# Performance work log

Hardware: AMD Instinct MI355X
Metric: run time of the kernel (lower is better)

The kernel has to match this reference:

```python
import jax, jax.numpy as jnp
import numpy as np

N_UNITS = 524288
BATCH = 16384


def setup_inputs() -> dict:
    key = jax.random.key(0)
    ks = jax.random.split(key, 10)
    left_feats = jax.random.normal(ks[0], (N_UNITS, 9), dtype=jnp.float32)
    right_feats = jax.random.normal(ks[1], (N_UNITS, 9), dtype=jnp.float32)
    left_seg = jnp.sort(jax.random.randint(ks[2], (N_UNITS,), 0, BATCH, dtype=jnp.int32))
    right_seg = jnp.sort(jax.random.randint(ks[3], (N_UNITS,), 0, BATCH, dtype=jnp.int32))
    W1 = jax.random.normal(ks[4], (9, 64), dtype=jnp.float32) * (1.0 / np.sqrt(9))
    b1 = jax.random.normal(ks[5], (64,), dtype=jnp.float32) * 0.01
    Wc1 = jax.random.normal(ks[6], (128, 32), dtype=jnp.float32) * (1.0 / np.sqrt(128))
    bc1 = jax.random.normal(ks[7], (32,), dtype=jnp.float32) * 0.01
    Wc2 = jax.random.normal(ks[8], (32, 1), dtype=jnp.float32) * (1.0 / np.sqrt(32))
    bc2 = jax.random.normal(ks[9], (1,), dtype=jnp.float32) * 0.01
    return {"left_feats": left_feats, "right_feats": right_feats,
            "left_seg": left_seg, "right_seg": right_seg,
            "W1": W1, "b1": b1, "Wc1": Wc1, "bc1": bc1, "Wc2": Wc2, "bc2": bc2}


def _pooled_features(feats, seg, W1, b1):
    # per-unit MLP 9 -> 64 with ReLU, then ragged sum-pool per instance
    h = jax.nn.relu(feats @ W1 + b1)                      # [N, 64]
    return jax.ops.segment_sum(h, seg, num_segments=BATCH)  # [B, 64]


def reference(left_feats, right_feats, left_seg, right_seg, W1, b1, Wc1, bc1, Wc2, bc2):
    left = _pooled_features(left_feats, left_seg, W1, b1)    # [B, 64]
    right = _pooled_features(right_feats, right_seg, W1, b1)  # [B, 64]
    combined = jnp.concatenate([left, right], axis=1)         # [B, 128]
    hidden = jax.nn.relu(combined @ Wc1 + bc1)                # [B, 32]
    logits = hidden @ Wc2 + bc2                               # [B, 1]
    return jax.nn.sigmoid(jnp.squeeze(logits, axis=-1))       # [B]
```

## Files before the change

### kernel.cpp

```cpp
#include <hip/hip_runtime.h>
#include <math.h>

#define BATCH_C 16384
#define SPW 2

typedef float f32x4  __attribute__((ext_vector_type(4)));
typedef f32x4 __attribute__((aligned(4))) f32x4_u;
typedef float f32x16 __attribute__((ext_vector_type(16)));
typedef short s16x8  __attribute__((ext_vector_type(8)));

static __device__ inline unsigned rlo_f(float x) {
    unsigned u = __float_as_uint(x);
    return (u + 0x7fffu + ((u >> 16) & 1u)) >> 16;
}
static __device__ inline unsigned rhi_f(float x) {
    unsigned u = __float_as_uint(x);
    return (u + 0x7fffu + ((u >> 16) & 1u)) & 0xffff0000u;
}

__global__ __launch_bounds__(256) void seg_starts_kernel(
    const int* __restrict__ lseg, const int* __restrict__ rseg, int n,
    int* __restrict__ lstart, int* __restrict__ rstart)
{
    const int* __restrict__ seg = blockIdx.y ? rseg : lseg;
    int* __restrict__ start = blockIdx.y ? rstart : lstart;
    int i = blockIdx.x * blockDim.x + threadIdx.x;
    if (i >= n) return;
    int s = seg[i];
    int prev = (i == 0) ? -1 : seg[i - 1];
    for (int b = prev + 1; b <= s; ++b) start[b] = i;
    if (i == n - 1) {
        for (int b = s + 1; b <= BATCH_C; ++b) start[b] = n;
    }
}

__global__ __launch_bounds__(256, 4) void fused_kernel(
    const float* __restrict__ lfeats, const float* __restrict__ rfeats,
    const int* __restrict__ lstart, const int* __restrict__ rstart,
    const float* __restrict__ W1, const float* __restrict__ b1,
    const float* __restrict__ Wc1, const float* __restrict__ bc1,
    const float* __restrict__ Wc2, const float* __restrict__ bc2,
    float* __restrict__ out, int nunits)
{
    const int lane = threadIdx.x & 63;
    const int wv   = threadIdx.x >> 6;
    const int S0   = (blockIdx.x * 4 + wv) * SPW;
    const int r    = lane & 31;
    const int hh   = lane >> 5;

    __shared__ __align__(16) short sBh[2][32][16];
    __shared__ __align__(16) short sBl[2][32][16];
    __shared__ __align__(16) float sWT[32 * 132];
    __shared__ float sb2[32];
    __shared__ float sw2v[32];
    __shared__ __align__(16) float rowbuf[4][SPW][128];

    {
        const int t    = threadIdx.x;
        const int tile = t >> 7;
        const int col  = (t >> 2) & 31;
        const int k0   = (t & 3) * 4;
        const int ch   = tile * 32 + col;
#pragma unroll
        for (int q = 0; q < 4; ++q) {
            const int k = k0 + q;
            float v = 0.0f;
            if (k < 9) v = W1[k * 64 + ch];
            else if (k == 9) v = b1[ch];
            unsigned hi = rlo_f(v);
            float d = v - __uint_as_float(hi << 16);
            sBh[tile][col][k] = (short)hi;
            sBl[tile][col][k] = (short)rlo_f(d);
        }
    }
    for (int idx = threadIdx.x; idx < 128 * 32; idx += 256) {
        sWT[(idx & 31) * 132 + (idx >> 5)] = Wc1[idx];
    }
    if (threadIdx.x < 32) {
        sb2[threadIdx.x]  = bc1[threadIdx.x];
        sw2v[threadIdx.x] = Wc2[threadIdx.x];
    }
    __syncthreads();

    const s16x8 bh0 = *reinterpret_cast<const s16x8*>(&sBh[0][r][hh * 8]);
    const s16x8 bh1 = *reinterpret_cast<const s16x8*>(&sBh[1][r][hh * 8]);
    const s16x8 bl0 = *reinterpret_cast<const s16x8*>(&sBl[0][r][hh * 8]);
    const s16x8 bl1 = *reinterpret_cast<const s16x8*>(&sBl[1][r][hh * 8]);

    const int bidx = S0 + (lane <= SPW ? lane : SPW);
    const int svl = lstart[bidx];
    const int svr = rstart[bidx];

#define FETCH(POS, P0,P1,P2,P3,P4,P5,P6,P7) do {                          \
        int u_ = (POS) + r; if (u_ > nunits - 1) u_ = nunits - 1;         \
        const float* fp_ = feats + (size_t)u_ * 9;                        \
        if (hh == 0) {                                                    \
            f32x4 x0_ = *reinterpret_cast<const f32x4_u*>(fp_);           \
            f32x4 x1_ = *reinterpret_cast<const f32x4_u*>(fp_ + 4);       \
            P0 = x0_.x; P1 = x0_.y; P2 = x0_.z; P3 = x0_.w;               \
            P4 = x1_.x; P5 = x1_.y; P6 = x1_.z; P7 = x1_.w;               \
        } else {                                                          \
            P0 = fp_[8];                                                  \
        }                                                                 \
    } while (0)

#define WINBODY(CNT, P0,P1,P2,P3,P4,P5,P6,P7) do {                        \
    unsigned u0_ = __float_as_uint(P0), u1_ = __float_as_uint(P1);        \
    unsigned u2_ = __float_as_uint(P2), u3_ = __float_as_uint(P3);        \
    unsigned u4_ = __float_as_uint(P4), u5_ = __float_as_uint(P5);        \
    unsigned u6_ = __float_as_uint(P6), u7_ = __float_as_uint(P7);        \
    float d0_ = P0 - __uint_as_float(u0_ & 0xffff0000u);                  \
    float d1_ = P1 - __uint_as_float(u1_ & 0xffff0000u);                  \
    float d2_ = P2 - __uint_as_float(u2_ & 0xffff0000u);                  \
    float d3_ = P3 - __uint_as_float(u3_ & 0xffff0000u);                  \
    float d4_ = P4 - __uint_as_float(u4_ & 0xffff0000u);                  \
    float d5_ = P5 - __uint_as_float(u5_ & 0xffff0000u);                  \
    float d6_ = P6 - __uint_as_float(u6_ & 0xffff0000u);                  \
    float d7_ = P7 - __uint_as_float(u7_ & 0xffff0000u);                  \
    unsigned H01_ = (u0_ >> 16) | (u1_ & 0xffff0000u);                    \
    unsigned H23_ = (u2_ >> 16) | (u3_ & 0xffff0000u);                    \
    unsigned H45_ = (u4_ >> 16) | (u5_ & 0xffff0000u);                    \
    unsigned H67_ = (u6_ >> 16) | (u7_ & 0xffff0000u);                    \
    unsigned L01_ = rlo_f(d0_) | rhi_f(d1_);                              \
    unsigned L23_ = rlo_f(d2_) | rhi_f(d3_);                              \
    unsigned L45_ = rlo_f(d4_) | rhi_f(d5_);                              \
    unsigned L67_ = rlo_f(d6_) | rhi_f(d7_);                              \
    const bool val_  = (r < (CNT));                                       \
    const bool keep_ = val_ && (hh == 0);                                 \
    unsigned HH01_ = hh ? ((u0_ >> 16) | 0x3F800000u) : H01_;             \
    unsigned LL01_ = hh ? rlo_f(d0_) : L01_;                              \
    HH01_ = val_ ? HH01_ : 0u;                                            \
    LL01_ = val_ ? LL01_ : 0u;                                            \
    unsigned HH23_ = keep_ ? H23_ : 0u, HH45_ = keep_ ? H45_ : 0u;        \
    unsigned HH67_ = keep_ ? H67_ : 0u;                                   \
    unsigned LL23_ = keep_ ? L23_ : 0u, LL45_ = keep_ ? L45_ : 0u;        \
    unsigned LL67_ = keep_ ? L67_ : 0u;                                   \
    union { unsigned u[4]; s16x8 v; } Ah_, Al_;                           \
    Ah_.u[0] = HH01_; Ah_.u[1] = HH23_; Ah_.u[2] = HH45_; Ah_.u[3] = HH67_;\
    Al_.u[0] = LL01_; Al_.u[1] = LL23_; Al_.u[2] = LL45_; Al_.u[3] = LL67_;\
    if (posN < end_abs) { FETCH(posN, P0,P1,P2,P3,P4,P5,P6,P7); }         \
    posN = segadv(posN);                                                  \
    f32x16 cc0 = (f32x16)0.0f, cc1 = (f32x16)0.0f;                        \
    cc0 = __builtin_amdgcn_mfma_f32_32x32x16_bf16(Al_.v, bh0, cc0, 0,0,0);\
    cc0 = __builtin_amdgcn_mfma_f32_32x32x16_bf16(Ah_.v, bl0, cc0, 0,0,0);\
    cc0 = __builtin_amdgcn_mfma_f32_32x32x16_bf16(Ah_.v, bh0, cc0, 0,0,0);\
    cc1 = __builtin_amdgcn_mfma_f32_32x32x16_bf16(Al_.v, bh1, cc1, 0,0,0);\
    cc1 = __builtin_amdgcn_mfma_f32_32x32x16_bf16(Ah_.v, bl1, cc1, 0,0,0);\
    cc1 = __builtin_amdgcn_mfma_f32_32x32x16_bf16(Ah_.v, bh1, cc1, 0,0,0);\
    float s0_ = 0.0f, s1_ = 0.0f;                                         \
    _Pragma("unroll")                                                     \
    for (int t_ = 0; t_ < 16; ++t_) {                                     \
        s0_ += fmaxf(cc0[t_], 0.0f);                                      \
        s1_ += fmaxf(cc1[t_], 0.0f);                                      \
    }                                                                     \
    acc0 += s0_; acc1 += s1_;                                             \
} while (0)

    for (int side = 0; side < 2; ++side) {
        const float* __restrict__ feats = side ? rfeats : lfeats;
        const int sv = side ? svr : svl;
        const int s_abs = __shfl(sv, 0, 64);
        const int e1v = __shfl(sv, 1, 64);
        const int e2v = __shfl(sv, 2, 64);
        const int end_abs = e2v;

        auto segadv = [&](int p) -> int {
            int se = (p >= e1v) ? e2v : e1v;
            int w = se - p; if (w > 32) w = 32;
            return (p >= end_abs) ? p : (p + w);
        };

        float A0=0,A1=0,A2=0,A3=0,A4=0,A5=0,A6=0,A7=0;
        float B0=0,B1=0,B2=0,B3=0,B4=0,B5=0,B6=0,B7=0;
        const int pa = s_abs;
        if (pa < end_abs) FETCH(pa, A0,A1,A2,A3,A4,A5,A6,A7);
        const int pb = segadv(pa);
        if (pb < end_abs) FETCH(pb, B0,B1,B2,B3,B4,B5,B6,B7);
        int posN = segadv(pb);

        float acc0 = 0.0f, acc1 = 0.0f;
        int parity = 0;
        int base = s_abs;
        const int earr[SPW] = {e1v, e2v};

#pragma unroll
        for (int c = 0; c < SPW; ++c) {
            const int ec = earr[c];
            while (base < ec) {
                int cnt = ec - base; if (cnt > 32) cnt = 32;
                if (parity == 0) { WINBODY(cnt, A0,A1,A2,A3,A4,A5,A6,A7); }
                else             { WINBODY(cnt, B0,B1,B2,B3,B4,B5,B6,B7); }
                parity ^= 1;
                base += cnt;
            }
            acc0 += __shfl_xor(acc0, 32, 64);
            acc1 += __shfl_xor(acc1, 32, 64);
            rowbuf[wv][c][side * 64 + lane] = hh ? acc1 : acc0;
            acc0 = 0.0f; acc1 = 0.0f;
        }
    }
#undef WINBODY
#undef FETCH

    asm volatile("s_waitcnt lgkmcnt(0)" ::: "memory");

    {
        const int j = lane & 31;
        const float* __restrict__ rb = &rowbuf[wv][hh][0];
        const float* __restrict__ wt = &sWT[j * 132];

        float accA = sb2[j], accB = 0.0f;
#pragma unroll 8
        for (int q = 0; q < 32; ++q) {
            f32x4 v = *reinterpret_cast<const f32x4*>(rb + q * 4);
            f32x4 w = *reinterpret_cast<const f32x4*>(wt + q * 4);
            accA = fmaf(v.x, w.x, accA);
            accB = fmaf(v.y, w.y, accB);
            accA = fmaf(v.z, w.z, accA);
            accB = fmaf(v.w, w.w, accB);
        }
        float hsv = fmaxf(accA + accB, 0.0f) * sw2v[j];
#pragma unroll
        for (int off = 16; off > 0; off >>= 1) hsv += __shfl_xor(hsv, off, 64);

        if (j == 0) {
            float logit = hsv + bc2[0];
            out[S0 + hh] = 1.0f / (1.0f + expf(-logit));
        }
    }
}

extern "C" void kernel_launch(void* const* d_in, const int* in_sizes, int n_in,
                              void* d_out, int out_size, void* d_ws, size_t ws_size,
                              hipStream_t stream)
{
    const float* lfeats = (const float*)d_in[0];
    const float* rfeats = (const float*)d_in[1];
    const int*   lseg   = (const int*)d_in[2];
    const int*   rseg   = (const int*)d_in[3];
    const float* W1     = (const float*)d_in[4];
    const float* b1     = (const float*)d_in[5];
    const float* Wc1    = (const float*)d_in[6];
    const float* bc1    = (const float*)d_in[7];
    const float* Wc2    = (const float*)d_in[8];
    const float* bc2    = (const float*)d_in[9];
    float* out = (float*)d_out;

    const int n = in_sizes[2];

    int* lstart = (int*)d_ws;
    int* rstart = lstart + (BATCH_C + 16);

    seg_starts_kernel<<<dim3((n + 255) / 256, 2), 256, 0, stream>>>(
        lseg, rseg, n, lstart, rstart);

    fused_kernel<<<BATCH_C / (SPW * 4), 256, 0, stream>>>(
        lfeats, rfeats, lstart, rstart, W1, b1, Wc1, bc1, Wc2, bc2, out, n);
}
```

Before: 40.25 us.

## Interleave left and right segment streams and use branch-free unit fetch

The previous code processed the left side and then the right side, double-buffering fetches within each. The new loop runs both sides at once, so each iteration issues two independent fetch and MFMA chains to hide load latency. It also makes the fetch branch-free with a per-lane offset load, splits the ReLU reduction into several partial sums, and lowers the launch_bounds occupancy hint from 4 to 2 to give the compiler more registers. The trade-off is more register pressure, possibly fewer resident waves per CU, and extra handling for sides and empty segments.

```diff
diff --git a/kernel.cpp b/kernel.cpp
--- a/kernel.cpp
+++ b/kernel.cpp
@@ -8,6 +8,8 @@
 typedef f32x4 __attribute__((aligned(4))) f32x4_u;
 typedef float f32x16 __attribute__((ext_vector_type(16)));
 typedef short s16x8  __attribute__((ext_vector_type(8)));
+
+typedef union { unsigned u[4]; s16x8 v; } abfrag_t;
 
 static __device__ inline unsigned rlo_f(float x) {
     unsigned u = __float_as_uint(x);
@@ -34,7 +36,7 @@
     }
 }
 
-__global__ __launch_bounds__(256, 4) void fused_kernel(
+__global__ __launch_bounds__(256, 2) void fused_kernel(
     const float* __restrict__ lfeats, const float* __restrict__ rfeats,
     const int* __restrict__ lstart, const int* __restrict__ rstart,
     const float* __restrict__ W1, const float* __restrict__ b1,
@@ -47,6 +49,8 @@
     const int S0   = (blockIdx.x * 4 + wv) * SPW;
     const int r    = lane & 31;
     const int hh   = lane >> 5;
+    const int nmax = nunits - 1;
+    const int ofs1 = hh ? 5 : 4;
 
     __shared__ __align__(16) short sBh[2][32][16];
     __shared__ __align__(16) short sBl[2][32][16];
@@ -87,120 +91,131 @@
     const s16x8 bl0 = *reinterpret_cast<const s16x8*>(&sBl[0][r][hh * 8]);
     const s16x8 bl1 = *reinterpret_cast<const s16x8*>(&sBl[1][r][hh * 8]);
 
+    const f32x16 kZ = (f32x16)0.0f;
+
+    rowbuf[wv][0][lane] = 0.0f;  rowbuf[wv][0][64 + lane] = 0.0f;
+    rowbuf[wv][1][lane] = 0.0f;  rowbuf[wv][1][64 + lane] = 0.0f;
+
     const int bidx = S0 + (lane <= SPW ? lane : SPW);
     const int svl = lstart[bidx];
     const int svr = rstart[bidx];
-
-#define FETCH(POS, P0,P1,P2,P3,P4,P5,P6,P7) do {                          \
-        int u_ = (POS) + r; if (u_ > nunits - 1) u_ = nunits - 1;         \
-        const float* fp_ = feats + (size_t)u_ * 9;                        \
-        if (hh == 0) {                                                    \
-            f32x4 x0_ = *reinterpret_cast<const f32x4_u*>(fp_);           \
-            f32x4 x1_ = *reinterpret_cast<const f32x4_u*>(fp_ + 4);       \
-            P0 = x0_.x; P1 = x0_.y; P2 = x0_.z; P3 = x0_.w;               \
-            P4 = x1_.x; P5 = x1_.y; P6 = x1_.z; P7 = x1_.w;               \
-        } else {                                                          \
-            P0 = fp_[8];                                                  \
-        }                                                                 \
+    const int sLv = __shfl(svl, 0, 64);
+    const int e1L = __shfl(svl, 1, 64);
+    const int e2L = __shfl(svl, 2, 64);
+    const int sRv = __shfl(svr, 0, 64);
+    const int e1R = __shfl(svr, 1, 64);
+    const int e2R = __shfl(svr, 2, 64);
+    const int endL = e2L, endR = e2R;
+
+#define FETCH_(F, POS, Q0,Q1,Q2,Q3,Q4,Q5,Q6,Q7) do {                      \
+        int u_ = (POS) + r; if (u_ > nmax) u_ = nmax;                     \
+        const float* fp_ = (F) + (size_t)u_ * 9;                          \
+        f32x4 x0_ = *reinterpret_cast<const f32x4_u*>(fp_);               \
+        f32x4 x1_ = *reinterpret_cast<const f32x4_u*>(fp_ + ofs1);        \
+        Q0 = hh ? x1_.w : x0_.x;                                          \
+        Q1 = x0_.y; Q2 = x0_.z; Q3 = x0_.w;                               \
+        Q4 = x1_.x; Q5 = x1_.y; Q6 = x1_.z; Q7 = x1_.w;                   \
     } while (0)
 
-#define WINBODY(CNT, P0,P1,P2,P3,P4,P5,P6,P7) do {                        \
-    unsigned u0_ = __float_as_uint(P0), u1_ = __float_as_uint(P1);        \
-    unsigned u2_ = __float_as_uint(P2), u3_ = __float_as_uint(P3);        \
-    unsigned u4_ = __float_as_uint(P4), u5_ = __float_as_uint(P5);        \
-    unsigned u6_ = __float_as_uint(P6), u7_ = __float_as_uint(P7);        \
-    float d0_ = P0 - __uint_as_float(u0_ & 0xffff0000u);                  \
-    float d1_ = P1 - __uint_as_float(u1_ & 0xffff0000u);                  \
-    float d2_ = P2 - __uint_as_float(u2_ & 0xffff0000u);                  \
-    float d3_ = P3 - __uint_as_float(u3_ & 0xffff0000u);                  \
-    float d4_ = P4 - __uint_as_float(u4_ & 0xffff0000u);                  \
-    float d5_ = P5 - __uint_as_float(u5_ & 0xffff0000u);                  \
-    float d6_ = P6 - __uint_as_float(u6_ & 0xffff0000u);                  \
-    float d7_ = P7 - __uint_as_float(u7_ & 0xffff0000u);                  \
-    unsigned H01_ = (u0_ >> 16) | (u1_ & 0xffff0000u);                    \
-    unsigned H23_ = (u2_ >> 16) | (u3_ & 0xffff0000u);                    \
-    unsigned H45_ = (u4_ >> 16) | (u5_ & 0xffff0000u);                    \
-    unsigned H67_ = (u6_ >> 16) | (u7_ & 0xffff0000u);                    \
-    unsigned L01_ = rlo_f(d0_) | rhi_f(d1_);                              \
-    unsigned L23_ = rlo_f(d2_) | rhi_f(d3_);                              \
-    unsigned L45_ = rlo_f(d4_) | rhi_f(d5_);                              \
-    unsigned L67_ = rlo_f(d6_) | rhi_f(d7_);                              \
-    const bool val_  = (r < (CNT));                                       \
-    const bool keep_ = val_ && (hh == 0);                                 \
-    unsigned HH01_ = hh ? ((u0_ >> 16) | 0x3F800000u) : H01_;             \
-    unsigned LL01_ = hh ? rlo_f(d0_) : L01_;                              \
-    HH01_ = val_ ? HH01_ : 0u;                                            \
-    LL01_ = val_ ? LL01_ : 0u;                                            \
-    unsigned HH23_ = keep_ ? H23_ : 0u, HH45_ = keep_ ? H45_ : 0u;        \
-    unsigned HH67_ = keep_ ? H67_ : 0u;                                   \
-    unsigned LL23_ = keep_ ? L23_ : 0u, LL45_ = keep_ ? L45_ : 0u;        \
-    unsigned LL67_ = keep_ ? L67_ : 0u;                                   \
-    union { unsigned u[4]; s16x8 v; } Ah_, Al_;                           \
-    Ah_.u[0] = HH01_; Ah_.u[1] = HH23_; Ah_.u[2] = HH45_; Ah_.u[3] = HH67_;\
-    Al_.u[0] = LL01_; Al_.u[1] = LL23_; Al_.u[2] = LL45_; Al_.u[3] = LL67_;\
-    if (posN < end_abs) { FETCH(posN, P0,P1,P2,P3,P4,P5,P6,P7); }         \
-    posN = segadv(posN);                                                  \
-    f32x16 cc0 = (f32x16)0.0f, cc1 = (f32x16)0.0f;                        \
-    cc0 = __builtin_amdgcn_mfma_f32_32x32x16_bf16(Al_.v, bh0, cc0, 0,0,0);\
-    cc0 = __builtin_amdgcn_mfma_f32_32x32x16_bf16(Ah_.v, bl0, cc0, 0,0,0);\
-    cc0 = __builtin_amdgcn_mfma_f32_32x32x16_bf16(Ah_.v, bh0, cc0, 0,0,0);\
-    cc1 = __builtin_amdgcn_mfma_f32_32x32x16_bf16(Al_.v, bh1, cc1, 0,0,0);\
-    cc1 = __builtin_amdgcn_mfma_f32_32x32x16_bf16(Ah_.v, bl1, cc1, 0,0,0);\
-    cc1 = __builtin_amdgcn_mfma_f32_32x32x16_bf16(Ah_.v, bh1, cc1, 0,0,0);\
-    float s0_ = 0.0f, s1_ = 0.0f;                                         \
+#define CONV_(Q0,Q1,Q2,Q3,Q4,Q5,Q6,Q7, CNT, AH, AL) do {                  \
+    unsigned u0_=__float_as_uint(Q0), u1_=__float_as_uint(Q1),            \
+             u2_=__float_as_uint(Q2), u3_=__float_as_uint(Q3),            \
+             u4_=__float_as_uint(Q4), u5_=__float_as_uint(Q5),            \
+             u6_=__float_as_uint(Q6), u7_=__float_as_uint(Q7);            \
+    float d0_=Q0-__uint_as_float(u0_&0xffff0000u);                        \
+    float d1_=Q1-__uint_as_float(u1_&0xffff0000u);                        \
+    float d2_=Q2-__uint_as_float(u2_&0xffff0000u);                        \
+    float d3_=Q3-__uint_as_float(u3_&0xffff0000u);                        \
+    float d4_=Q4-__uint_as_float(u4_&0xffff0000u);                        \
+    float d5_=Q5-__uint_as_float(u5_&0xffff0000u);                        \
+    float d6_=Q6-__uint_as_float(u6_&0xffff0000u);                        \
+    float d7_=Q7-__uint_as_float(u7_&0xffff0000u);                        \
+    unsigned h01_=(u0_>>16)|(hh?0x3F800000u:(u1_&0xffff0000u));           \
+    unsigned l01_=rlo_f(d0_)|(hh?0u:rhi_f(d1_));                          \
+    unsigned h23_=(u2_>>16)|(u3_&0xffff0000u);                            \
+    unsigned h45_=(u4_>>16)|(u5_&0xffff0000u);                            \
+    unsigned h67_=(u6_>>16)|(u7_&0xffff0000u);                            \
+    unsigned l23_=rlo_f(d2_)|rhi_f(d3_);                                  \
+    unsigned l45_=rlo_f(d4_)|rhi_f(d5_);                                  \
+    unsigned l67_=rlo_f(d6_)|rhi_f(d7_);                                  \
+    const bool v_ = (r < (CNT));                                          \
+    const bool k_ = v_ && (hh == 0);                                      \
+    AH.u[0]=v_?h01_:0u; AL.u[0]=v_?l01_:0u;                               \
+    AH.u[1]=k_?h23_:0u; AL.u[1]=k_?l23_:0u;                               \
+    AH.u[2]=k_?h45_:0u; AL.u[2]=k_?l45_:0u;                               \
+    AH.u[3]=k_?h67_:0u; AL.u[3]=k_?l67_:0u;                               \
+} while (0)
+
+#define MFMAEPI_(AH, AL, A0, A1) do {                                     \
+    f32x16 c0_ = __builtin_amdgcn_mfma_f32_32x32x16_bf16(AL.v, bh0, kZ, 0,0,0); \
+    c0_ = __builtin_amdgcn_mfma_f32_32x32x16_bf16(AH.v, bl0, c0_, 0,0,0); \
+    c0_ = __builtin_amdgcn_mfma_f32_32x32x16_bf16(AH.v, bh0, c0_, 0,0,0); \
+    f32x16 c1_ = __builtin_amdgcn_mfma_f32_32x32x16_bf16(AL.v, bh1, kZ, 0,0,0); \
+    c1_ = __builtin_amdgcn_mfma_f32_32x32x16_bf16(AH.v, bl1, c1_, 0,0,0); \
+    c1_ = __builtin_amdgcn_mfma_f32_32x32x16_bf16(AH.v, bh1, c1_, 0,0,0); \
+    float sA_=0.f,sB_=0.f,sC_=0.f,sD_=0.f,tA_=0.f,tB_=0.f,tC_=0.f,tD_=0.f;\
     _Pragma("unroll")                                                     \
-    for (int t_ = 0; t_ < 16; ++t_) {                                     \
-        s0_ += fmaxf(cc0[t_], 0.0f);                                      \
-        s1_ += fmaxf(cc1[t_], 0.0f);                                      \
+    for (int t_=0; t_<4; ++t_) {                                          \
+        sA_+=fmaxf(c0_[t_],0.f);    sB_+=fmaxf(c0_[t_+4],0.f);            \
+        sC_+=fmaxf(c0_[t_+8],0.f);  sD_+=fmaxf(c0_[t_+12],0.f);           \
+        tA_+=fmaxf(c1_[t_],0.f);    tB_+=fmaxf(c1_[t_+4],0.f);            \
+        tC_+=fmaxf(c1_[t_+8],0.f);  tD_+=fmaxf(c1_[t_+12],0.f);           \
     }                                                                     \
-    acc0 += s0_; acc1 += s1_;                                             \
-} while (0)
-
-    for (int side = 0; side < 2; ++side) {
-        const float* __restrict__ feats = side ? rfeats : lfeats;
-        const int sv = side ? svr : svl;
-        const int s_abs = __shfl(sv, 0, 64);
-        const int e1v = __shfl(sv, 1, 64);
-        const int e2v = __shfl(sv, 2, 64);
-        const int end_abs = e2v;
-
-        auto segadv = [&](int p) -> int {
-            int se = (p >= e1v) ? e2v : e1v;
-            int w = se - p; if (w > 32) w = 32;
-            return (p >= end_abs) ? p : (p + w);
-        };
-
-        float A0=0,A1=0,A2=0,A3=0,A4=0,A5=0,A6=0,A7=0;
-        float B0=0,B1=0,B2=0,B3=0,B4=0,B5=0,B6=0,B7=0;
-        const int pa = s_abs;
-        if (pa < end_abs) FETCH(pa, A0,A1,A2,A3,A4,A5,A6,A7);
-        const int pb = segadv(pa);
-        if (pb < end_abs) FETCH(pb, B0,B1,B2,B3,B4,B5,B6,B7);
-        int posN = segadv(pb);
-
-        float acc0 = 0.0f, acc1 = 0.0f;
-        int parity = 0;
-        int base = s_abs;
-        const int earr[SPW] = {e1v, e2v};
-
-#pragma unroll
-        for (int c = 0; c < SPW; ++c) {
-            const int ec = earr[c];
-            while (base < ec) {
-                int cnt = ec - base; if (cnt > 32) cnt = 32;
-                if (parity == 0) { WINBODY(cnt, A0,A1,A2,A3,A4,A5,A6,A7); }
-                else             { WINBODY(cnt, B0,B1,B2,B3,B4,B5,B6,B7); }
-                parity ^= 1;
-                base += cnt;
-            }
-            acc0 += __shfl_xor(acc0, 32, 64);
-            acc1 += __shfl_xor(acc1, 32, 64);
-            rowbuf[wv][c][side * 64 + lane] = hh ? acc1 : acc0;
-            acc0 = 0.0f; acc1 = 0.0f;
-        }
-    }
-#undef WINBODY
-#undef FETCH
+    A0 += (sA_+sB_)+(sC_+sD_);                                            \
+    A1 += (tA_+tB_)+(tC_+tD_);                                            \
+} while (0)
+
+#define STEP_(S) do {                                                     \
+    int cnt_ = ec##S - base##S; if (cnt_ > 32) cnt_ = 32;                 \
+    abfrag_t AH_, AL_;                                                    \
+    CONV_(p0##S,p1##S,p2##S,p3##S,p4##S,p5##S,p6##S,p7##S, cnt_, AH_, AL_);\
+    int nxt_ = base##S + cnt_;                                            \
+    int fpos_ = (nxt_ < end##S) ? nxt_ : 0;  \
+    FETCH_(f##S, fpos_, p0##S,p1##S,p2##S,p3##S,p4##S,p5##S,p6##S,p7##S); \
+    MFMAEPI_(AH_, AL_, ac0##S, ac1##S);                                   \
+    base##S = nxt_;                                                       \
+} while (0)
+
+#define FLUSH_(S, SIDEOFS) do {                                           \
+    if (base##S >= ec##S) {                                               \
+        ac0##S += __shfl_xor(ac0##S, 32, 64);                             \
+        ac1##S += __shfl_xor(ac1##S, 32, 64);                             \
+        if (cs##S < SPW)                                                  \
+            rowbuf[wv][cs##S][(SIDEOFS) + lane] = hh ? ac1##S : ac0##S;   \
+        ac0##S = 0.0f; ac1##S = 0.0f;                                     \
+        ++cs##S; ec##S = e2##S;                                           \
+    }                                                                     \
+} while (0)
+
+    const float* __restrict__ fL = lfeats;
+    const float* __restrict__ fR = rfeats;
+    int baseL = sLv, baseR = sRv;
+    int csL, ecL, csR, ecR;
+    if (baseL >= e1L) { csL = 1; ecL = e2L; } else { csL = 0; ecL = e1L; }
+    if (baseR >= e1R) { csR = 1; ecR = e2R; } else { csR = 0; ecR = e1R; }
+    float ac0L = 0.f, ac1L = 0.f, ac0R = 0.f, ac1R = 0.f;
+    float p0L=0,p1L=0,p2L=0,p3L=0,p4L=0,p5L=0,p6L=0,p7L=0;
+    float p0R=0,p1R=0,p2R=0,p3R=0,p4R=0,p5R=0,p6R=0,p7R=0;
+
+    if (baseL < endL) FETCH_(fL, baseL, p0L,p1L,p2L,p3L,p4L,p5L,p6L,p7L);
+    if (baseR < endR) FETCH_(fR, baseR, p0R,p1R,p2R,p3R,p4R,p5R,p6R,p7R);
+
+    bool aL = baseL < endL, aR = baseR < endR;
+    while (aL && aR) {
+        STEP_(L);
+        STEP_(R);
+        FLUSH_(L, 0);
+        FLUSH_(R, 64);
+        aL = baseL < endL; aR = baseR < endR;
+    }
+    while (aL) { STEP_(L); FLUSH_(L, 0);  aL = baseL < endL; }
+    while (aR) { STEP_(R); FLUSH_(R, 64); aR = baseR < endR; }
+
+#undef FLUSH_
+#undef STEP_
+#undef MFMAEPI_
+#undef CONV_
+#undef FETCH_
 
     asm volatile("s_waitcnt lgkmcnt(0)" ::: "memory");
 
```

Result: faster. 36.41 us, median of 2 (-9.5%).
